# Performance work log

Measured on AMD Instinct MI355X. Metric: run time of the kernel, lower is better.

The kernel has to match this reference:

```python
import jax, jax.numpy as jnp
import numpy as np

N = 20000      # nodes
E = 640000     # edges
H = 128        # hidden_channels
F = 128        # num_filters
G = 50         # num_gaussians
L = 6          # num_interactions
CUT = 10.0     # cutoff
NG = 64        # num graphs in batch
NODE_CLASS = 100


def ssp(x):
    # ShiftedSoftplus: softplus(x) - log(2)
    return jax.nn.softplus(x) - jnp.asarray(np.log(2.0), x.dtype)


def setup_inputs() -> dict:
    key = jax.random.key(0)
    ks = jax.random.split(key, 20)
    z = jax.random.randint(ks[0], (N,), 0, NODE_CLASS)
    pos = jax.random.normal(ks[1], (N, 3), dtype=jnp.float32) * 3.0
    edge_index = jax.random.randint(ks[2], (2, E), 0, N)
    batch = jnp.sort(jax.random.randint(ks[3], (N,), 0, NG))
    s = 0.05
    emb = jax.random.normal(ks[4], (NODE_CLASS, H), dtype=jnp.float32) * s
    mlp_w1 = jax.random.normal(ks[5], (L, G, F), dtype=jnp.float32) * s
    mlp_b1 = jnp.zeros((L, F), jnp.float32)
    mlp_w2 = jax.random.normal(ks[6], (L, F, F), dtype=jnp.float32) * s
    mlp_b2 = jnp.zeros((L, F), jnp.float32)
    conv_w1 = jax.random.normal(ks[7], (L, H, F), dtype=jnp.float32) * s
    conv_w2 = jax.random.normal(ks[8], (L, F, H), dtype=jnp.float32) * s
    conv_b2 = jnp.zeros((L, H), jnp.float32)
    lin_w = jax.random.normal(ks[9], (L, H, H), dtype=jnp.float32) * s
    lin_b = jnp.zeros((L, H), jnp.float32)
    out1_w = jax.random.normal(ks[10], (H, H), dtype=jnp.float32) * s
    out1_b = jnp.zeros((H,), jnp.float32)
    out2_w = jax.random.normal(ks[11], (H, H), dtype=jnp.float32) * s
    out2_b = jnp.zeros((H,), jnp.float32)
    return dict(z=z, pos=pos, edge_index=edge_index, batch=batch, emb=emb,
                mlp_w1=mlp_w1, mlp_b1=mlp_b1, mlp_w2=mlp_w2, mlp_b2=mlp_b2,
                conv_w1=conv_w1, conv_w2=conv_w2, conv_b2=conv_b2,
                lin_w=lin_w, lin_b=lin_b,
                out1_w=out1_w, out1_b=out1_b, out2_w=out2_w, out2_b=out2_b)


def reference(z, pos, edge_index, batch, emb,
              mlp_w1, mlp_b1, mlp_w2, mlp_b2,
              conv_w1, conv_w2, conv_b2, lin_w, lin_b,
              out1_w, out1_b, out2_w, out2_b):
    src, dst = edge_index[0], edge_index[1]  # x_j = x[src], aggregate at dst
    h = emb[z]                               # [N, H]
    d = jnp.linalg.norm(pos[src] - pos[dst], axis=-1)  # [E]
    # GaussianSmearing(0, cutoff, G)
    offset = jnp.linspace(0.0, CUT, G).astype(d.dtype)
    coeff = -0.5 / (offset[1] - offset[0]) ** 2
    edge_attr = jnp.exp(coeff * (d[:, None] - offset[None, :]) ** 2)  # [E, G]
    # cosine cutoff
    C = 0.5 * (jnp.cos(d * jnp.pi / CUT) + 1.0)  # [E]
    n = h.shape[0]
    for l in range(L):
        # edge filter: mlp(edge_attr) * C
        W = ssp(edge_attr @ mlp_w1[l] + mlp_b1[l]) @ mlp_w2[l] + mlp_b2[l]
        W = W * C[:, None]                      # [E, F]
        xf = h @ conv_w1[l]                     # lin1, no bias: [N, F]
        msg = xf[src] * W                       # gather + weight
        agg = jax.ops.segment_sum(msg, dst, num_segments=n)  # scatter-add
        x = agg @ conv_w2[l] + conv_b2[l]       # lin2
        x = ssp(x)
        x = x @ lin_w[l] + lin_b[l]
        h = h + x                               # residual
    h = ssp(h @ out1_w + out1_b) @ out2_w + out2_b
    # readout = 'mean'
    sums = jax.ops.segment_sum(h, batch, num_segments=NG)
    cnt = jax.ops.segment_sum(jnp.ones((n,), h.dtype), batch, num_segments=NG)
    return sums / jnp.maximum(cnt, 1.0)[:, None]
```

## Files before the change

### kernel.cpp

```cpp
#include <hip/hip_runtime.h>
#include <math.h>

#define NN 20000
#define NE 640000
#define GDIM 50
#define LAYERS 6
#define NGRAPH 64
#define TBL 2048
#define DMAXF 12.8f
#define G2_PAD 136

typedef __attribute__((ext_vector_type(8))) short short8;
typedef __attribute__((ext_vector_type(4))) float floatx4;

__device__ __forceinline__ float sspf(float x) {
    float sp = (x > 30.0f) ? x : log1pf(expf(x));
    return sp - 0.69314718055994530942f;
}

__device__ __forceinline__ unsigned short f2bs(float f) {
    union { float f; unsigned int i; } u; u.f = f;
    unsigned int r = u.i + 0x7fffu + ((u.i >> 16) & 1u);
    return (unsigned short)(r >> 16);
}

__device__ __forceinline__ float bs2f(unsigned int bits16) {
    union { unsigned int i; float f; } u; u.i = bits16 << 16;
    return u.f;
}

__device__ __forceinline__ short8 pack_bf16x8(float4 a, float4 b) {
    short8 o;
    o[0] = (short)f2bs(a.x); o[1] = (short)f2bs(a.y);
    o[2] = (short)f2bs(a.z); o[3] = (short)f2bs(a.w);
    o[4] = (short)f2bs(b.x); o[5] = (short)f2bs(b.y);
    o[6] = (short)f2bs(b.z); o[7] = (short)f2bs(b.w);
    return o;
}

struct WArgs { const float* s[26]; unsigned short* d[26]; };
#define PREP_WBLK 416
__global__ void prep_a(WArgs a, int* __restrict__ deg,
                       float* __restrict__ A_tab, const int* __restrict__ z,
                       const float* __restrict__ emb, float* __restrict__ h) {
    __shared__ float tile[32][33];
    int b = blockIdx.x;
    if (b < PREP_WBLK) {
        int mz = b >> 4, sub = b & 15;
        int bx = (sub & 3) * 32, by = (sub >> 2) * 32;
        const float* Wm = a.s[mz];
        unsigned short* Wo = a.d[mz];
        int tx = threadIdx.x & 31, ty = threadIdx.x >> 5;
        for (int r = ty; r < 32; r += 8) tile[r][tx] = Wm[(by + r) * 128 + bx + tx];
        __syncthreads();
        for (int r = ty; r < 32; r += 8) Wo[(bx + r) * 128 + by + tx] = f2bs(tile[tx][r]);
        return;
    }
    int idx = (b - PREP_WBLK) * 256 + threadIdx.x;
    if (idx < NN) { deg[idx] = 0; return; }
    idx -= NN;
    if (idx < (TBL + 2) * GDIM) {
        int i = idx / GDIM, g = idx % GDIM;
        float v = 0.0f;
        if (i <= TBL) {
            float d = (float)i * (DMAXF / (float)TBL);
            float step = 10.0f / 49.0f;
            float off = (float)g * step;
            float coeff = -0.5f / (step * step);
            float dd = d - off;
            v = expf(coeff * dd * dd);
        }
        A_tab[idx] = v;
        return;
    }
    idx -= (TBL + 2) * GDIM;
    if (idx < NN * 32) {
        int n = idx >> 5, q = idx & 31;
        ((float4*)h)[n * 32 + q] = ((const float4*)emb)[(size_t)z[n] * 32 + q];
    }
}

__global__ void deg_hist(const int* __restrict__ dst, int* __restrict__ deg) {
    int j = blockIdx.x * blockDim.x + threadIdx.x;
    if (j >= NE) return;
    atomicAdd(&deg[dst[j]], 1);
}

__global__ void scan_a(const int* __restrict__ deg, int* __restrict__ row_ptr,
                       int* __restrict__ bsum) {
    __shared__ int sh[256];
    int b = blockIdx.x, t = threadIdx.x;
    int i = b * 256 + t;
    int v = (i < NN) ? deg[i] : 0;
    int x = v;
    sh[t] = x;
    __syncthreads();
    for (int off = 1; off < 256; off <<= 1) {
        int u = (t >= off) ? sh[t - off] : 0;
        __syncthreads();
        x += u;
        sh[t] = x;
        __syncthreads();
    }
    if (i <= NN) row_ptr[i] = x - v;
    if (t == 255) bsum[b] = x;
}

__global__ void scan_b(const int* __restrict__ bsum, int* __restrict__ row_ptr,
                       int* __restrict__ cursor) {
    __shared__ int spref;
    int b = blockIdx.x, t = threadIdx.x;
    if (t < 64) {
        int s = 0;
        if (t < b) s += bsum[t];
        if (t + 64 < b) s += bsum[t + 64];
        for (int off = 32; off; off >>= 1) s += __shfl_down(s, off);
        if (t == 0) spref = s;
    }
    __syncthreads();
    int prefix = spref;
    int i = b * 256 + t;
    if (i < NN) {
        int v = row_ptr[i] + prefix;
        row_ptr[i] = v;
        cursor[i] = v;
    }
    if (b == 0 && t == 0) row_ptr[NN] = NE;
}

__global__ void csr_fill(const float* __restrict__ pos, const int* __restrict__ src,
                         const int* __restrict__ dst, int* __restrict__ cursor,
                         int2* __restrict__ csr) {
    int j = blockIdx.x * blockDim.x + threadIdx.x;
    if (j >= NE) return;
    int s = src[j], tno = dst[j];
    float dx = pos[3*s+0] - pos[3*tno+0];
    float dy = pos[3*s+1] - pos[3*tno+1];
    float dz = pos[3*s+2] - pos[3*tno+2];
    float d = sqrtf(dx*dx + dy*dy + dz*dz);
    float u = d * ((float)TBL / DMAXF);
    u = fminf(u, (float)(TBL + 1));
    int i0 = (int)u; if (i0 > TBL) i0 = TBL;
    float f = u - (float)i0;
    int p = atomicAdd(&cursor[tno], 1);
    csr[p] = make_int2((i0 << 15) | s, __float_as_int(f));
}

template <int K>
__launch_bounds__(256, 2)
__global__ void gemm_t(const float* __restrict__ A, const float* __restrict__ W,
                       const float* __restrict__ bias, float* __restrict__ Y, int M,
                       int act, int aStride, int wStride, int bStride, int yStride) {
    constexpr int KP = (K + 3) & ~3;
    __shared__ __align__(16) float Ws[KP * 128];
    __shared__ __align__(16) float As[32 * KP];
    int l = blockIdx.y;
    A += (size_t)l * aStride;
    W += (size_t)l * wStride;
    if (bias) bias += (size_t)l * bStride;
    Y += (size_t)l * yStride;
    int t = threadIdx.x;
    int row0 = blockIdx.x * 32;
    for (int i = t; i < KP * 128; i += 256) Ws[i] = (i < K * 128) ? W[i] : 0.0f;
    for (int i = t; i < 32 * KP; i += 256) {
        int r = i / KP, k = i % KP;
        float v = 0.f;
        if (k < K && row0 + r < M) v = A[(size_t)(row0 + r) * K + k];
        As[r * KP + k] = v;
    }
    __syncthreads();
    int tx = t & 31, ty = t >> 5;
    int c0 = tx * 4, r0 = ty * 4;
    float acc[4][4] = {{0.f}};
    #pragma unroll 4
    for (int k = 0; k < KP; k += 4) {
        float4 a0 = *(const float4*)&As[(r0 + 0) * KP + k];
        float4 a1 = *(const float4*)&As[(r0 + 1) * KP + k];
        float4 a2 = *(const float4*)&As[(r0 + 2) * KP + k];
        float4 a3 = *(const float4*)&As[(r0 + 3) * KP + k];
        float4 w0 = *(const float4*)&Ws[(k + 0) * 128 + c0];
        float4 w1 = *(const float4*)&Ws[(k + 1) * 128 + c0];
        float4 w2 = *(const float4*)&Ws[(k + 2) * 128 + c0];
        float4 w3 = *(const float4*)&Ws[(k + 3) * 128 + c0];
        float av[4][4] = {{a0.x,a0.y,a0.z,a0.w},{a1.x,a1.y,a1.z,a1.w},
                          {a2.x,a2.y,a2.z,a2.w},{a3.x,a3.y,a3.z,a3.w}};
        float wv[4][4] = {{w0.x,w0.y,w0.z,w0.w},{w1.x,w1.y,w1.z,w1.w},
                          {w2.x,w2.y,w2.z,w2.w},{w3.x,w3.y,w3.z,w3.w}};
        #pragma unroll
        for (int i = 0; i < 4; i++)
            #pragma unroll
            for (int j = 0; j < 4; j++)
                #pragma unroll
                for (int q = 0; q < 4; q++)
                    acc[i][j] += av[i][q] * wv[q][j];
    }
    float b0 = 0.f, b1 = 0.f, b2 = 0.f, b3 = 0.f;
    if (bias) { b0 = bias[c0]; b1 = bias[c0+1]; b2 = bias[c0+2]; b3 = bias[c0+3]; }
    #pragma unroll
    for (int i = 0; i < 4; i++) {
        int r = row0 + r0 + i;
        if (r >= M) break;
        float4 v;
        v.x = acc[i][0] + b0; v.y = acc[i][1] + b1; v.z = acc[i][2] + b2; v.w = acc[i][3] + b3;
        if (act == 1) { v.x = sspf(v.x); v.y = sspf(v.y); v.z = sspf(v.z); v.w = sspf(v.w); }
        *(float4*)&Y[(size_t)r * 128 + c0] = v;
    }
}

__launch_bounds__(256)
__global__ void gemm_cs2(const float* __restrict__ A1, const unsigned short* __restrict__ W1t,
                         const float* __restrict__ bias1, float* __restrict__ Y1, int M1,
                         const float* __restrict__ A2, const unsigned short* __restrict__ W2t,
                         unsigned short* __restrict__ Yb2, int M2) {
    int y = blockIdx.y;
    const float* A; const unsigned short* Wt; const float* bias;
    float* Yf; unsigned short* Yb; int M;
    if (y < LAYERS) {
        M = M1;
        A = A1 + (size_t)y * M1 * 128;
        Wt = W1t + (size_t)y * 16384;
        bias = bias1 + (size_t)y * 128;
        Yf = Y1 + (size_t)y * M1 * 128;
        Yb = nullptr;
    } else {
        M = M2; A = A2; Wt = W2t; bias = nullptr; Yf = nullptr; Yb = Yb2;
    }
    int wv = threadIdx.x >> 6, lane = threadIdx.x & 63;
    int row0 = blockIdx.x * 32;
    if (row0 >= M) return;
    int lm = lane & 15, lk = (lane >> 4) * 8, orow = (lane >> 4) * 4;
    int r0 = row0 + lm;      r0 = (r0 < M) ? r0 : M - 1;
    int r1 = row0 + 16 + lm; r1 = (r1 < M) ? r1 : M - 1;
    const float* Ap0 = A + (size_t)r0 * 128;
    const float* Ap1 = A + (size_t)r1 * 128;
    short8 af0[4], af1[4];
    #pragma unroll
    for (int kq = 0; kq < 4; kq++) {
        af0[kq] = pack_bf16x8(*(const float4*)(Ap0 + kq * 32 + lk),
                              *(const float4*)(Ap0 + kq * 32 + lk + 4));
        af1[kq] = pack_bf16x8(*(const float4*)(Ap1 + kq * 32 + lk),
                              *(const float4*)(Ap1 + kq * 32 + lk + 4));
    }
    floatx4 acc[2][2];
    #pragma unroll
    for (int i = 0; i < 2; i++)
        #pragma unroll
        for (int j = 0; j < 2; j++) acc[i][j] = (floatx4){0, 0, 0, 0};
    const unsigned short* Wp = Wt + (size_t)(wv * 32) * 128;
    #pragma unroll
    for (int kq = 0; kq < 4; kq++) {
        #pragma unroll
        for (int ct = 0; ct < 2; ct++) {
            short8 bf = *(const short8*)(Wp + (size_t)(ct * 16 + lm) * 128 + kq * 32 + lk);
            acc[0][ct] = __builtin_amdgcn_mfma_f32_16x16x32_bf16(af0[kq], bf, acc[0][ct], 0, 0, 0);
            acc[1][ct] = __builtin_amdgcn_mfma_f32_16x16x32_bf16(af1[kq], bf, acc[1][ct], 0, 0, 0);
        }
    }
    #pragma unroll
    for (int tt = 0; tt < 2; tt++) {
        #pragma unroll
        for (int ct = 0; ct < 2; ct++) {
            int c = wv * 32 + ct * 16 + lm;
            float b = bias ? bias[c] : 0.f;
            #pragma unroll
            for (int r = 0; r < 4; r++) {
                int rr = row0 + tt * 16 + orow + r;
                if (rr >= M) continue;
                float v = acc[tt][ct][r] + b;
                if (Yf) Yf[(size_t)rr * 128 + c] = v;
                if (Yb) Yb[(size_t)rr * 128 + c] = f2bs(v);
            }
        }
    }
}

__launch_bounds__(256)
__global__ void layer_k(const int* __restrict__ row_ptr, const int2* __restrict__ csr,
                        const unsigned int* __restrict__ Tb,
                        const unsigned short* __restrict__ xfb_in,
                        const unsigned short* __restrict__ W2t, const float* __restrict__ b2,
                        const unsigned short* __restrict__ W3t, const float* __restrict__ b3,
                        float* __restrict__ h,
                        const unsigned short* __restrict__ W1nt,
                        unsigned short* __restrict__ xfb_out) {
    __shared__ unsigned short Ls[16 * G2_PAD];
    int wv = threadIdx.x >> 6, lane = threadIdx.x & 63;
    int row0 = blockIdx.x * 16;
    int lm = lane & 15, lk = (lane >> 4) * 8, orow = (lane >> 4) * 4;
    int cw = wv * 32;
    float rpre[2][4];
    #pragma unroll
    for (int ct = 0; ct < 2; ct++)
        #pragma unroll
        for (int r = 0; r < 4; r++)
            rpre[ct][r] = h[(size_t)(row0 + orow + r) * 128 + cw + ct * 16 + lm];
    {
        const uint2* Tb2 = (const uint2*)Tb;
        const unsigned int* xf32 = (const unsigned int*)xfb_in;
        #pragma unroll
        for (int nn = 0; nn < 4; nn++) {
            int n = row0 + wv * 4 + nn;
            int e0 = __builtin_amdgcn_readfirstlane(row_ptr[n]);
            int e1 = __builtin_amdgcn_readfirstlane(row_ptr[n + 1]);
            float a0 = 0.f, a1 = 0.f;
            int e = e0;
            for (; e + 8 <= e1; e += 8) {
                unsigned int px[8]; float ff[8];
                #pragma unroll
                for (int q = 0; q < 8; q++) {
                    int2 ed = csr[e + q];
                    px[q] = (unsigned int)__builtin_amdgcn_readfirstlane(ed.x);
                    ff[q] = __int_as_float(__builtin_amdgcn_readfirstlane(ed.y));
                }
                uint2 tw[8]; unsigned int xv[8];
                #pragma unroll
                for (int q = 0; q < 8; q++) {
                    tw[q] = Tb2[(size_t)(px[q] >> 15) * 64 + lane];
                    xv[q] = xf32[(size_t)(px[q] & 0x7fffu) * 64 + lane];
                }
                #pragma unroll
                for (int q = 0; q < 8; q++) {
                    float w0 = bs2f(tw[q].x & 0xffffu), d0 = bs2f(tw[q].x >> 16);
                    float w1 = bs2f(tw[q].y & 0xffffu), d1 = bs2f(tw[q].y >> 16);
                    float x0 = bs2f(xv[q] & 0xffffu), x1 = bs2f(xv[q] >> 16);
                    a0 = fmaf(x0, fmaf(ff[q], d0, w0), a0);
                    a1 = fmaf(x1, fmaf(ff[q], d1, w1), a1);
                }
            }
            for (; e < e1; e++) {
                int2 ed = csr[e];
                unsigned int px = (unsigned int)__builtin_amdgcn_readfirstlane(ed.x);
                float f = __int_as_float(__builtin_amdgcn_readfirstlane(ed.y));
                uint2 tw = Tb2[(size_t)(px >> 15) * 64 + lane];
                unsigned int xv = xf32[(size_t)(px & 0x7fffu) * 64 + lane];
                float w0 = bs2f(tw.x & 0xffffu), d0 = bs2f(tw.x >> 16);
                float w1 = bs2f(tw.y & 0xffffu), d1 = bs2f(tw.y >> 16);
                float x0 = bs2f(xv & 0xffffu), x1 = bs2f(xv >> 16);
                a0 = fmaf(x0, fmaf(f, d0, w0), a0);
                a1 = fmaf(x1, fmaf(f, d1, w1), a1);
            }
            unsigned int pk = ((unsigned)f2bs(a1) << 16) | f2bs(a0);
            *(unsigned int*)&Ls[(wv * 4 + nn) * G2_PAD + 2 * lane] = pk;
        }
    }
    __syncthreads();
    {
        short8 af[4];
        #pragma unroll
        for (int kq = 0; kq < 4; kq++)
            af[kq] = *(const short8*)&Ls[lm * G2_PAD + kq * 32 + lk];
        __syncthreads();
        floatx4 acc[2];
        acc[0] = (floatx4){0, 0, 0, 0}; acc[1] = (floatx4){0, 0, 0, 0};
        const unsigned short* Wp = W2t + (size_t)cw * 128;
        #pragma unroll
        for (int kq = 0; kq < 4; kq++) {
            #pragma unroll
            for (int ct = 0; ct < 2; ct++) {
                short8 bf = *(const short8*)(Wp + (size_t)(ct * 16 + lm) * 128 + kq * 32 + lk);
                acc[ct] = __builtin_amdgcn_mfma_f32_16x16x32_bf16(af[kq], bf, acc[ct], 0, 0, 0);
            }
        }
        #pragma unroll
        for (int ct = 0; ct < 2; ct++) {
            int c = cw + ct * 16 + lm;
            float b = b2[c];
            #pragma unroll
            for (int r = 0; r < 4; r++)
                Ls[(orow + r) * G2_PAD + c] = f2bs(sspf(acc[ct][r] + b));
        }
    }
    __syncthreads();
    float vout[2][4];
    {
        short8 a2[4];
        #pragma unroll
        for (int kq = 0; kq < 4; kq++)
            a2[kq] = *(const short8*)&Ls[lm * G2_PAD + kq * 32 + lk];
        floatx4 acc[2];
        acc[0] = (floatx4){0, 0, 0, 0}; acc[1] = (floatx4){0, 0, 0, 0};
        const unsigned short* Wp = W3t + (size_t)cw * 128;
        #pragma unroll
        for (int kq = 0; kq < 4; kq++) {
            #pragma unroll
            for (int ct = 0; ct < 2; ct++) {
                short8 bf = *(const short8*)(Wp + (size_t)(ct * 16 + lm) * 128 + kq * 32 + lk);
                acc[ct] = __builtin_amdgcn_mfma_f32_16x16x32_bf16(a2[kq], bf, acc[ct], 0, 0, 0);
            }
        }
        #pragma unroll
        for (int ct = 0; ct < 2; ct++) {
            int c = cw + ct * 16 + lm;
            float b = b3[c];
            #pragma unroll
            for (int r = 0; r < 4; r++) {
                int rr = row0 + orow + r;
                float v = acc[ct][r] + b + rpre[ct][r];
                h[(size_t)rr * 128 + c] = v;
                vout[ct][r] = v;
            }
        }
    }
    if (!W1nt) return;
    __syncthreads();
    #pragma unroll
    for (int ct = 0; ct < 2; ct++) {
        int c = cw + ct * 16 + lm;
        #pragma unroll
        for (int r = 0; r < 4; r++)
            Ls[(orow + r) * G2_PAD + c] = f2bs(vout[ct][r]);
    }
    __syncthreads();
    {
        short8 a3[4];
        #pragma unroll
        for (int kq = 0; kq < 4; kq++)
            a3[kq] = *(const short8*)&Ls[lm * G2_PAD + kq * 32 + lk];
        floatx4 acc[2];
        acc[0] = (floatx4){0, 0, 0, 0}; acc[1] = (floatx4){0, 0, 0, 0};
        const unsigned short* Wp = W1nt + (size_t)cw * 128;
        #pragma unroll
        for (int kq = 0; kq < 4; kq++) {
            #pragma unroll
            for (int ct = 0; ct < 2; ct++) {
                short8 bf = *(const short8*)(Wp + (size_t)(ct * 16 + lm) * 128 + kq * 32 + lk);
                acc[ct] = __builtin_amdgcn_mfma_f32_16x16x32_bf16(a3[kq], bf, acc[ct], 0, 0, 0);
            }
        }
        #pragma unroll
        for (int ct = 0; ct < 2; ct++) {
            int c = cw + ct * 16 + lm;
            #pragma unroll
            for (int r = 0; r < 4; r++)
                xfb_out[(size_t)(row0 + orow + r) * 128 + c] = f2bs(acc[ct][r]);
        }
    }
}

__launch_bounds__(256)
__global__ void gemm3h(const float* __restrict__ A,
                       const unsigned short* __restrict__ W2t, const float* __restrict__ b2,
                       const unsigned short* __restrict__ W3t, const float* __restrict__ b3,
                       float* __restrict__ Yf) {
    __shared__ unsigned short Ls[16 * G2_PAD];
    int wv = threadIdx.x >> 6, lane = threadIdx.x & 63;
    int row0 = blockIdx.x * 16;
    int lm = lane & 15, lk = (lane >> 4) * 8, orow = (lane >> 4) * 4;
    int cw = wv * 32;
    {
        const float* Ap = A + (size_t)(row0 + lm) * 128;
        short8 af[4];
        #pragma unroll
        for (int kq = 0; kq < 4; kq++)
            af[kq] = pack_bf16x8(*(const float4*)(Ap + kq * 32 + lk),
                                 *(const float4*)(Ap + kq * 32 + lk + 4));
        floatx4 acc[2];
        acc[0] = (floatx4){0, 0, 0, 0}; acc[1] = (floatx4){0, 0, 0, 0};
        const unsigned short* Wp = W2t + (size_t)cw * 128;
        #pragma unroll
        for (int kq = 0; kq < 4; kq++) {
            #pragma unroll
            for (int ct = 0; ct < 2; ct++) {
                short8 bf = *(const short8*)(Wp + (size_t)(ct * 16 + lm) * 128 + kq * 32 + lk);
                acc[ct] = __builtin_amdgcn_mfma_f32_16x16x32_bf16(af[kq], bf, acc[ct], 0, 0, 0);
            }
        }
        #pragma unroll
        for (int ct = 0; ct < 2; ct++) {
            int c = cw + ct * 16 + lm;
            float b = b2[c];
            #pragma unroll
            for (int r = 0; r < 4; r++)
                Ls[(orow + r) * G2_PAD + c] = f2bs(sspf(acc[ct][r] + b));
        }
    }
    __syncthreads();
    {
        short8 a2[4];
        #pragma unroll
        for (int kq = 0; kq < 4; kq++)
            a2[kq] = *(const short8*)&Ls[lm * G2_PAD + kq * 32 + lk];
        floatx4 acc[2];
        acc[0] = (floatx4){0, 0, 0, 0}; acc[1] = (floatx4){0, 0, 0, 0};
        const unsigned short* Wp = W3t + (size_t)cw * 128;
        #pragma unroll
        for (int kq = 0; kq < 4; kq++) {
            #pragma unroll
            for (int ct = 0; ct < 2; ct++) {
                short8 bf = *(const short8*)(Wp + (size_t)(ct * 16 + lm) * 128 + kq * 32 + lk);
                acc[ct] = __builtin_amdgcn_mfma_f32_16x16x32_bf16(a2[kq], bf, acc[ct], 0, 0, 0);
            }
        }
        #pragma unroll
        for (int ct = 0; ct < 2; ct++) {
            int c = cw + ct * 16 + lm;
            float b = b3[c];
            #pragma unroll
            for (int r = 0; r < 4; r++)
                Yf[(size_t)(row0 + orow + r) * 128 + c] = acc[ct][r] + b;
        }
    }
}

__global__ void tquant(const float* __restrict__ T, unsigned int* __restrict__ Tb) {
    int idx = blockIdx.x * blockDim.x + threadIdx.x;
    const int total = LAYERS * (TBL + 1) * 128;
    if (idx >= total) return;
    int c = idx & 127;
    int li = idx >> 7;
    int i = li % (TBL + 1);
    int l = li / (TBL + 1);
    float d0 = (float)i * (DMAXF / (float)TBL);
    float d1 = (float)(i + 1) * (DMAXF / (float)TBL);
    float C0 = 0.5f * (cosf(d0 * 0.31415926535897931f) + 1.0f);
    float C1 = 0.5f * (cosf(d1 * 0.31415926535897931f) + 1.0f);
    const float* row = T + ((size_t)l * (TBL + 2) + i) * 128 + c;
    float w = row[0] * C0;
    float nw = row[128] * C1;
    Tb[idx] = ((unsigned)f2bs(nw - w) << 16) | f2bs(w);
}

__global__ void readout(const float* __restrict__ hout, const int* __restrict__ batch,
                        float* __restrict__ out) {
    int g = blockIdx.x;
    int t = threadIdx.x;
    int c = t & 127, half = t >> 7;
    __shared__ int sh[2];
    __shared__ float red[128];
    if (t < 2) {
        int target = g + t;
        int lo = 0, hi = NN;
        while (lo < hi) {
            int mid = (lo + hi) >> 1;
            if (batch[mid] < target) lo = mid + 1; else hi = mid;
        }
        sh[t] = lo;
    }
    __syncthreads();
    int lo = sh[0], hi = sh[1];
    float s = 0.f;
    for (int n = lo + half; n < hi; n += 2) s += hout[(size_t)n * 128 + c];
    if (half == 1) red[c] = s;
    __syncthreads();
    if (half == 0) {
        int cnt = hi - lo;
        out[g * 128 + c] = (s + red[c]) / (float)(cnt > 0 ? cnt : 1);
    }
}

extern "C" void kernel_launch(void* const* d_in, const int* in_sizes, int n_in,
                              void* d_out, int out_size, void* d_ws, size_t ws_size,
                              hipStream_t stream) {
    const int*   z       = (const int*)d_in[0];
    const float* pos     = (const float*)d_in[1];
    const int*   eidx    = (const int*)d_in[2];
    const int*   src     = eidx;
    const int*   dst     = eidx + NE;
    const int*   batch   = (const int*)d_in[3];
    const float* emb     = (const float*)d_in[4];
    const float* mlp_w1  = (const float*)d_in[5];
    const float* mlp_b1  = (const float*)d_in[6];
    const float* mlp_w2  = (const float*)d_in[7];
    const float* mlp_b2  = (const float*)d_in[8];
    const float* conv_w1 = (const float*)d_in[9];
    const float* conv_w2 = (const float*)d_in[10];
    const float* conv_b2 = (const float*)d_in[11];
    const float* lin_w   = (const float*)d_in[12];
    const float* lin_b   = (const float*)d_in[13];
    const float* out1_w  = (const float*)d_in[14];
    const float* out1_b  = (const float*)d_in[15];
    const float* out2_w  = (const float*)d_in[16];
    const float* out2_b  = (const float*)d_in[17];
    float* out = (float*)d_out;

    char* wp = (char*)d_ws;
    auto alloc = [&](size_t bytes) {
        char* p = wp;
        wp += (bytes + 255) & ~(size_t)255;
        return p;
    };
    const int Mt = TBL + 2;
    int*    deg     = (int*)alloc(NN * 4);
    int*    row_ptr = (int*)alloc((NN + 1) * 4);
    int*    cursor  = (int*)alloc(NN * 4);
    int*    bsum    = (int*)alloc(128 * 4);
    int2*   csr     = (int2*)alloc((size_t)NE * 8);
    float*  A_tab   = (float*)alloc((size_t)Mt * GDIM * 4);
    float*  T1all   = (float*)alloc((size_t)LAYERS * Mt * 128 * 4);
    float*  T       = (float*)alloc((size_t)LAYERS * Mt * 128 * 4);
    unsigned int* Tb = (unsigned int*)alloc((size_t)LAYERS * (TBL + 1) * 128 * 4);
    float*  h       = (float*)alloc((size_t)NN * 128 * 4);
    float*  hout    = (float*)alloc((size_t)NN * 128 * 4);
    unsigned short* xfb = (unsigned short*)alloc((size_t)NN * 128 * 2);
    unsigned short* wbf = (unsigned short*)alloc((size_t)26 * 16384 * 2);
    unsigned short* mlp_w2t  = wbf;
    unsigned short* conv_w1t = wbf + (size_t)6 * 16384;
    unsigned short* conv_w2t = wbf + (size_t)12 * 16384;
    unsigned short* lin_wt   = wbf + (size_t)18 * 16384;
    unsigned short* out1_wt  = wbf + (size_t)24 * 16384;
    unsigned short* out2_wt  = wbf + (size_t)25 * 16384;

    WArgs wa;
    for (int l = 0; l < 6; l++) {
        wa.s[l]      = mlp_w2  + (size_t)l * 16384;  wa.d[l]      = mlp_w2t  + (size_t)l * 16384;
        wa.s[6 + l]  = conv_w1 + (size_t)l * 16384;  wa.d[6 + l]  = conv_w1t + (size_t)l * 16384;
        wa.s[12 + l] = conv_w2 + (size_t)l * 16384;  wa.d[12 + l] = conv_w2t + (size_t)l * 16384;
        wa.s[18 + l] = lin_w   + (size_t)l * 16384;  wa.d[18 + l] = lin_wt   + (size_t)l * 16384;
    }
    wa.s[24] = out1_w; wa.d[24] = out1_wt;
    wa.s[25] = out2_w; wa.d[25] = out2_wt;
    const int initN = NN + Mt * GDIM + NN * 32;
    prep_a<<<PREP_WBLK + (initN + 255) / 256, 256, 0, stream>>>(wa, deg, A_tab, z, emb, h);

    deg_hist<<<(NE + 255) / 256, 256, 0, stream>>>(dst, deg);
    const int NB = (NN + 255) / 256;
    scan_a<<<NB, 256, 0, stream>>>(deg, row_ptr, bsum);
    scan_b<<<NB, 256, 0, stream>>>(bsum, row_ptr, cursor);
    csr_fill<<<(NE + 255) / 256, 256, 0, stream>>>(pos, src, dst, cursor, csr);

    const int gt32 = (Mt + 31) / 32;
    gemm_t<GDIM><<<dim3(gt32, LAYERS), 256, 0, stream>>>(
        A_tab, mlp_w1, mlp_b1, T1all, Mt, 1, 0, GDIM * 128, 128, Mt * 128);
    gemm_cs2<<<dim3(NN / 32, LAYERS + 1), 256, 0, stream>>>(
        T1all, mlp_w2t, mlp_b2, T, Mt,
        h, conv_w1t, xfb, NN);
    tquant<<<(LAYERS * (TBL + 1) * 128 + 255) / 256, 256, 0, stream>>>(T, Tb);

    const int gn = NN / 16;
    for (int l = 0; l < LAYERS; l++) {
        const unsigned short* w1n = (l + 1 < LAYERS) ? conv_w1t + (size_t)(l + 1) * 16384 : nullptr;
        layer_k<<<gn, 256, 0, stream>>>(row_ptr, csr,
                                        Tb + (size_t)l * (TBL + 1) * 128, xfb,
                                        conv_w2t + (size_t)l * 16384, conv_b2 + l * 128,
                                        lin_wt + (size_t)l * 16384, lin_b + l * 128,
                                        h, w1n, xfb);
    }

    gemm3h<<<gn, 256, 0, stream>>>(h, out1_wt, out1_b, out2_wt, out2_b, hout);
    readout<<<NGRAPH, 256, 0, stream>>>(hout, batch, out);
}
```

Measured before the change: 576.8 us.

## Split fused layer kernel into per-node edge aggregation and dense GEMM kernel

The fused per-layer kernel is split in two. A new edge_agg kernel gives each destination node a 256-thread block, in which two waves split the 128 channels and two edge parities share the edge list; the partial sums are reduced through shared memory and written as bf16 aggregates. A separate gemm3 kernel reads those aggregates and runs the conv_w2, lin and next-layer conv_w1 MFMA GEMMs. The aim is to expose more parallelism and shorten the serial gather chain, which was latency-bound with one wave looping over four nodes. The cost is an extra launch per layer, a round trip of the aggregate buffer through global memory, and narrower per-lane gather loads. It also removes the in-place read/write of xfb across blocks in the old fused kernel.

```diff
diff --git a/kernel.cpp b/kernel.cpp
--- a/kernel.cpp
+++ b/kernel.cpp
@@ -275,14 +275,11 @@
 }
 
 __launch_bounds__(256)
-__global__ void layer_k(const int* __restrict__ row_ptr, const int2* __restrict__ csr,
-                        const unsigned int* __restrict__ Tb,
-                        const unsigned short* __restrict__ xfb_in,
-                        const unsigned short* __restrict__ W2t, const float* __restrict__ b2,
-                        const unsigned short* __restrict__ W3t, const float* __restrict__ b3,
-                        float* __restrict__ h,
-                        const unsigned short* __restrict__ W1nt,
-                        unsigned short* __restrict__ xfb_out) {
+__global__ void gemm3(const unsigned short* __restrict__ aggb,
+                      const unsigned short* __restrict__ W2t, const float* __restrict__ b2,
+                      const unsigned short* __restrict__ W3t, const float* __restrict__ b3,
+                      const float* __restrict__ resid, float* __restrict__ Yf,
+                      const unsigned short* __restrict__ W1nt, unsigned short* __restrict__ xfb) {
     __shared__ unsigned short Ls[16 * G2_PAD];
     int wv = threadIdx.x >> 6, lane = threadIdx.x & 63;
     int row0 = blockIdx.x * 16;
@@ -293,63 +290,13 @@
     for (int ct = 0; ct < 2; ct++)
         #pragma unroll
         for (int r = 0; r < 4; r++)
-            rpre[ct][r] = h[(size_t)(row0 + orow + r) * 128 + cw + ct * 16 + lm];
+            rpre[ct][r] = resid[(size_t)(row0 + orow + r) * 128 + cw + ct * 16 + lm];
     {
-        const uint2* Tb2 = (const uint2*)Tb;
-        const unsigned int* xf32 = (const unsigned int*)xfb_in;
-        #pragma unroll
-        for (int nn = 0; nn < 4; nn++) {
-            int n = row0 + wv * 4 + nn;
-            int e0 = __builtin_amdgcn_readfirstlane(row_ptr[n]);
-            int e1 = __builtin_amdgcn_readfirstlane(row_ptr[n + 1]);
-            float a0 = 0.f, a1 = 0.f;
-            int e = e0;
-            for (; e + 8 <= e1; e += 8) {
-                unsigned int px[8]; float ff[8];
-                #pragma unroll
-                for (int q = 0; q < 8; q++) {
-                    int2 ed = csr[e + q];
-                    px[q] = (unsigned int)__builtin_amdgcn_readfirstlane(ed.x);
-                    ff[q] = __int_as_float(__builtin_amdgcn_readfirstlane(ed.y));
-                }
-                uint2 tw[8]; unsigned int xv[8];
-                #pragma unroll
-                for (int q = 0; q < 8; q++) {
-                    tw[q] = Tb2[(size_t)(px[q] >> 15) * 64 + lane];
-                    xv[q] = xf32[(size_t)(px[q] & 0x7fffu) * 64 + lane];
-                }
-                #pragma unroll
-                for (int q = 0; q < 8; q++) {
-                    float w0 = bs2f(tw[q].x & 0xffffu), d0 = bs2f(tw[q].x >> 16);
-                    float w1 = bs2f(tw[q].y & 0xffffu), d1 = bs2f(tw[q].y >> 16);
-                    float x0 = bs2f(xv[q] & 0xffffu), x1 = bs2f(xv[q] >> 16);
-                    a0 = fmaf(x0, fmaf(ff[q], d0, w0), a0);
-                    a1 = fmaf(x1, fmaf(ff[q], d1, w1), a1);
-                }
-            }
-            for (; e < e1; e++) {
-                int2 ed = csr[e];
-                unsigned int px = (unsigned int)__builtin_amdgcn_readfirstlane(ed.x);
-                float f = __int_as_float(__builtin_amdgcn_readfirstlane(ed.y));
-                uint2 tw = Tb2[(size_t)(px >> 15) * 64 + lane];
-                unsigned int xv = xf32[(size_t)(px & 0x7fffu) * 64 + lane];
-                float w0 = bs2f(tw.x & 0xffffu), d0 = bs2f(tw.x >> 16);
-                float w1 = bs2f(tw.y & 0xffffu), d1 = bs2f(tw.y >> 16);
-                float x0 = bs2f(xv & 0xffffu), x1 = bs2f(xv >> 16);
-                a0 = fmaf(x0, fmaf(f, d0, w0), a0);
-                a1 = fmaf(x1, fmaf(f, d1, w1), a1);
-            }
-            unsigned int pk = ((unsigned)f2bs(a1) << 16) | f2bs(a0);
-            *(unsigned int*)&Ls[(wv * 4 + nn) * G2_PAD + 2 * lane] = pk;
-        }
-    }
-    __syncthreads();
-    {
+        const unsigned short* Ap = aggb + (size_t)(row0 + lm) * 128;
         short8 af[4];
         #pragma unroll
         for (int kq = 0; kq < 4; kq++)
-            af[kq] = *(const short8*)&Ls[lm * G2_PAD + kq * 32 + lk];
-        __syncthreads();
+            af[kq] = *(const short8*)(Ap + kq * 32 + lk);
         floatx4 acc[2];
         acc[0] = (floatx4){0, 0, 0, 0}; acc[1] = (floatx4){0, 0, 0, 0};
         const unsigned short* Wp = W2t + (size_t)cw * 128;
@@ -396,7 +343,7 @@
             for (int r = 0; r < 4; r++) {
                 int rr = row0 + orow + r;
                 float v = acc[ct][r] + b + rpre[ct][r];
-                h[(size_t)rr * 128 + c] = v;
+                Yf[(size_t)rr * 128 + c] = v;
                 vout[ct][r] = v;
             }
         }
@@ -432,7 +379,7 @@
             int c = cw + ct * 16 + lm;
             #pragma unroll
             for (int r = 0; r < 4; r++)
-                xfb_out[(size_t)(row0 + orow + r) * 128 + c] = f2bs(acc[ct][r]);
+                xfb[(size_t)(row0 + orow + r) * 128 + c] = f2bs(acc[ct][r]);
         }
     }
 }
@@ -518,6 +465,56 @@
     float w = row[0] * C0;
     float nw = row[128] * C1;
     Tb[idx] = ((unsigned)f2bs(nw - w) << 16) | f2bs(w);
+}
+
+__launch_bounds__(256)
+__global__ void edge_agg(const int* __restrict__ row_ptr, const int2* __restrict__ csr,
+                         const unsigned int* __restrict__ Tb,
+                         const unsigned short* __restrict__ xfb,
+                         unsigned short* __restrict__ aggb) {
+    __shared__ float red[128];
+    int wv = __builtin_amdgcn_readfirstlane(threadIdx.x >> 6);
+    int lane = threadIdx.x & 63;
+    int n = blockIdx.x;
+    int c = (wv & 1) * 64 + lane;
+    int par = wv >> 1;
+    int e0 = row_ptr[n], e1 = row_ptr[n + 1];
+    float ax = 0.f;
+    int e = e0 + par;
+    for (; e + 14 < e1; e += 16) {
+        unsigned int px[8]; float ff[8];
+        #pragma unroll
+        for (int q = 0; q < 8; q++) {
+            int2 ed = csr[e + 2 * q];
+            px[q] = (unsigned int)__builtin_amdgcn_readfirstlane(ed.x);
+            ff[q] = __int_as_float(__builtin_amdgcn_readfirstlane(ed.y));
+        }
+        unsigned int tw[8]; unsigned short xv[8];
+        #pragma unroll
+        for (int q = 0; q < 8; q++) {
+            tw[q] = Tb[(px[q] >> 15) * 128 + c];
+            xv[q] = xfb[(size_t)(px[q] & 0x7fffu) * 128 + c];
+        }
+        #pragma unroll
+        for (int q = 0; q < 8; q++) {
+            float w = bs2f(tw[q] & 0xffffu), dw = bs2f(tw[q] >> 16);
+            float x = bs2f((unsigned int)xv[q]);
+            ax = fmaf(x, fmaf(ff[q], dw, w), ax);
+        }
+    }
+    for (; e < e1; e += 2) {
+        int2 ed = csr[e];
+        unsigned int px = (unsigned int)__builtin_amdgcn_readfirstlane(ed.x);
+        float f = __int_as_float(__builtin_amdgcn_readfirstlane(ed.y));
+        unsigned int tw = Tb[(px >> 15) * 128 + c];
+        unsigned short xv = xfb[(size_t)(px & 0x7fffu) * 128 + c];
+        float w = bs2f(tw & 0xffffu), dw = bs2f(tw >> 16);
+        float x = bs2f((unsigned int)xv);
+        ax = fmaf(x, fmaf(f, dw, w), ax);
+    }
+    if (par == 1) red[c] = ax;
+    __syncthreads();
+    if (par == 0) aggb[(size_t)n * 128 + c] = f2bs(ax + red[c]);
 }
 
 __global__ void readout(const float* __restrict__ hout, const int* __restrict__ batch,
@@ -591,8 +588,9 @@
     unsigned int* Tb = (unsigned int*)alloc((size_t)LAYERS * (TBL + 1) * 128 * 4);
     float*  h       = (float*)alloc((size_t)NN * 128 * 4);
     float*  hout    = (float*)alloc((size_t)NN * 128 * 4);
-    unsigned short* xfb = (unsigned short*)alloc((size_t)NN * 128 * 2);
-    unsigned short* wbf = (unsigned short*)alloc((size_t)26 * 16384 * 2);
+    unsigned short* aggb = (unsigned short*)alloc((size_t)NN * 128 * 2);
+    unsigned short* xfb  = (unsigned short*)alloc((size_t)NN * 128 * 2);
+    unsigned short* wbf  = (unsigned short*)alloc((size_t)26 * 16384 * 2);
     unsigned short* mlp_w2t  = wbf;
     unsigned short* conv_w1t = wbf + (size_t)6 * 16384;
     unsigned short* conv_w2t = wbf + (size_t)12 * 16384;
@@ -628,12 +626,12 @@
 
     const int gn = NN / 16;
     for (int l = 0; l < LAYERS; l++) {
+        edge_agg<<<NN, 256, 0, stream>>>(row_ptr, csr,
+                                         Tb + (size_t)l * (TBL + 1) * 128, xfb, aggb);
         const unsigned short* w1n = (l + 1 < LAYERS) ? conv_w1t + (size_t)(l + 1) * 16384 : nullptr;
-        layer_k<<<gn, 256, 0, stream>>>(row_ptr, csr,
-                                        Tb + (size_t)l * (TBL + 1) * 128, xfb,
-                                        conv_w2t + (size_t)l * 16384, conv_b2 + l * 128,
-                                        lin_wt + (size_t)l * 16384, lin_b + l * 128,
-                                        h, w1n, xfb);
+        gemm3<<<gn, 256, 0, stream>>>(aggb, conv_w2t + (size_t)l * 16384, conv_b2 + l * 128,
+                                      lin_wt + (size_t)l * 16384, lin_b + l * 128,
+                                      h, h, w1n, xfb);
     }
 
     gemm3h<<<gn, 256, 0, stream>>>(h, out1_wt, out1_b, out2_wt, out2_b, hout);
```

After: 632.4 us. +9.6%, slower.
